# Kernel optimization log

Hardware: AMD Instinct MI355X
Metric: run time of the kernel (lower is better)

The kernel has to match this reference:

```python
import jax, jax.numpy as jnp
import numpy as np

B, S, D, H, DFF = 4, 2048, 2048, 16, 8192
DH = D // H
THETA = 10000.0
EPS = 1e-5


def rmsnorm(x, g):
    return x * jax.lax.rsqrt(jnp.mean(x * x, axis=-1, keepdims=True) + EPS) * g


def rope(x, pos):
    # x: [B, H, S, DH]; rotate interleaved even/odd pairs
    half = DH // 2
    inv_freq = THETA ** (-(jnp.arange(half, dtype=jnp.float32) * 2.0) / DH)  # [half]
    ang = pos.astype(jnp.float32)[:, None] * inv_freq  # [S, half]
    cos, sin = jnp.cos(ang), jnp.sin(ang)
    x1, x2 = x[..., 0::2], x[..., 1::2]
    r1 = x1 * cos - x2 * sin
    r2 = x1 * sin + x2 * cos
    return jnp.stack([r1, r2], axis=-1).reshape(x.shape)


def setup_inputs() -> dict:
    key = jax.random.key(0)
    ks = jax.random.split(key, 12)
    s = 0.02
    return {
        "x": jax.random.normal(ks[0], (B, S, D), dtype=jnp.float32),
        "attention_mask": jnp.ones((S, S), dtype=bool),
        "wq": jax.random.normal(ks[1], (D, D), dtype=jnp.float32) * s,
        "wk": jax.random.normal(ks[2], (D, D), dtype=jnp.float32) * s,
        "wv": jax.random.normal(ks[3], (D, D), dtype=jnp.float32) * s,
        "wo": jax.random.normal(ks[4], (D, D), dtype=jnp.float32) * s,
        "w1": jax.random.normal(ks[5], (DFF, D), dtype=jnp.float32) * s,
        "w2": jax.random.normal(ks[6], (D, DFF), dtype=jnp.float32) * s,
        "w3": jax.random.normal(ks[7], (DFF, D), dtype=jnp.float32) * s,
        "g1": jnp.ones((D,), dtype=jnp.float32),
        "g2": jnp.ones((D,), dtype=jnp.float32),
    }


def reference(x, attention_mask, wq, wk, wv, wo, w1, w2, w3, g1, g2):
    pos = jnp.arange(x.shape[-2])
    # pre-norm attention
    h = rmsnorm(x, g1)
    q = (h @ wq.T).reshape(B, S, H, DH).transpose(0, 2, 1, 3)
    k = (h @ wk.T).reshape(B, S, H, DH).transpose(0, 2, 1, 3)
    v = (h @ wv.T).reshape(B, S, H, DH).transpose(0, 2, 1, 3)
    q = rope(q, pos)
    k = rope(k, pos)
    scores = jnp.einsum("bhqd,bhkd->bhqk", q, k) / np.float32(np.sqrt(DH))
    scores = jnp.where(attention_mask, scores, jnp.float32(-1e9))
    attn = jax.nn.softmax(scores, axis=-1)
    o = jnp.einsum("bhqk,bhkd->bhqd", attn, v)
    o = o.transpose(0, 2, 1, 3).reshape(B, S, D) @ wo.T
    x = x + o
    # pre-norm SwiGLU FFN
    h2 = rmsnorm(x, g2)
    ffn = (jax.nn.silu(h2 @ w1.T) * (h2 @ w3.T)) @ w2.T
    return x + ffn
```

## Files before the change

### kernel.cpp

```cpp
#include <hip/hip_runtime.h>
#include <cstdint>
#include <cstddef>

#define B_   4
#define S_   2048
#define D_   2048
#define H_   16
#define DH_  128
#define DFF_ 8192
#define LOG2E 1.4426950408889634f

typedef __bf16 bf16_t;
typedef __bf16 bf16x4 __attribute__((ext_vector_type(4)));
typedef __bf16 bf16x8 __attribute__((ext_vector_type(8)));
typedef float  f32x4  __attribute__((ext_vector_type(4)));

#define MFMA16 __builtin_amdgcn_mfma_f32_16x16x32_bf16

__device__ __forceinline__ void glds16(const void* g, void* l) {
  __builtin_amdgcn_global_load_lds((__attribute__((address_space(1))) void*)g,
                                   (__attribute__((address_space(3))) void*)l,
                                   16, 0, 0);
}

__global__ __launch_bounds__(256) void cvt_kernel(const float* __restrict__ in,
                                                  bf16_t* __restrict__ out, int n8) {
  int i = blockIdx.x * 256 + threadIdx.x;
  if (i >= n8) return;
  const float4* p4 = (const float4*)in;
  float4 a = p4[2 * (size_t)i];
  float4 b = p4[2 * (size_t)i + 1];
  bf16x8 o;
  o[0] = (bf16_t)a.x; o[1] = (bf16_t)a.y; o[2] = (bf16_t)a.z; o[3] = (bf16_t)a.w;
  o[4] = (bf16_t)b.x; o[5] = (bf16_t)b.y; o[6] = (bf16_t)b.z; o[7] = (bf16_t)b.w;
  ((bf16x8*)out)[i] = o;
}

__global__ __launch_bounds__(256) void rmsnorm_kernel(const float* __restrict__ x,
                                                      const float* __restrict__ g,
                                                      bf16_t* __restrict__ out) {
  const int row = blockIdx.x, tid = threadIdx.x;
  const float* xr = x + (size_t)row * D_;
  float4 a = ((const float4*)xr)[tid * 2];
  float4 b = ((const float4*)xr)[tid * 2 + 1];
  float ss = a.x*a.x + a.y*a.y + a.z*a.z + a.w*a.w
           + b.x*b.x + b.y*b.y + b.z*b.z + b.w*b.w;
#pragma unroll
  for (int m = 1; m < 64; m <<= 1) ss += __shfl_xor(ss, m);
  __shared__ float red[4];
  if ((tid & 63) == 0) red[tid >> 6] = ss;
  __syncthreads();
  float tot = red[0] + red[1] + red[2] + red[3];
  float rms = rsqrtf(tot * (1.0f / D_) + 1e-5f);
  float4 ga = ((const float4*)g)[tid * 2];
  float4 gb = ((const float4*)g)[tid * 2 + 1];
  bf16x8 o;
  o[0] = (bf16_t)(a.x * rms * ga.x); o[1] = (bf16_t)(a.y * rms * ga.y);
  o[2] = (bf16_t)(a.z * rms * ga.z); o[3] = (bf16_t)(a.w * rms * ga.w);
  o[4] = (bf16_t)(b.x * rms * gb.x); o[5] = (bf16_t)(b.y * rms * gb.y);
  o[6] = (bf16_t)(b.z * rms * gb.z); o[7] = (bf16_t)(b.w * rms * gb.w);
  ((bf16x8*)out)[(size_t)row * 256 + tid] = o;
}


#define Q_RD_A(d, mg)                                                         \
  do {                                                                        \
    const char* p_ = ldsb + (d) * 32768 + (wm * 128 + (mg) * 64 + l15) * 128; \
    _Pragma("unroll") for (int i_ = 0; i_ < 4; i_++) {                        \
      afr[i_][0] = *(const bf16x8*)(p_ + i_ * 2048 + acol0);                  \
      afr[i_][1] = *(const bf16x8*)(p_ + i_ * 2048 + acol1);                  \
    }                                                                         \
  } while (0)

#define Q_RD_B(dst, d, ng)                                                    \
  do {                                                                        \
    const char* p_ = ldsb + 65536 + (d) * 32768 +                             \
                     (wn * 64 + (ng) * 32 + l15) * 128;                       \
    _Pragma("unroll") for (int j_ = 0; j_ < 2; j_++) {                        \
      dst[j_][0] = *(const bf16x8*)(p_ + j_ * 2048 + acol0);                  \
      dst[j_][1] = *(const bf16x8*)(p_ + j_ * 2048 + acol1);                  \
    }                                                                         \
  } while (0)

#define Q_STAGE_A(d, kt)                                                      \
  do {                                                                        \
    char* dst_ = ldsb + (d) * 32768 + o0;                                     \
    const bf16_t* s_ = Asrc + (size_t)(kt) * 64;                              \
    glds16(s_, dst_);                                                         \
    glds16(s_ + 64 * (size_t)K, dst_ + 8192);                                 \
    glds16(s_ + 128 * (size_t)K, dst_ + 16384);                               \
    glds16(s_ + 192 * (size_t)K, dst_ + 24576);                               \
  } while (0)

#define Q_STAGE_B(d, kt)                                                      \
  do {                                                                        \
    char* dst_ = ldsb + 65536 + (d) * 32768 + o0;                             \
    const bf16_t* s_ = Wsrc + (size_t)(kt) * 64;                              \
    glds16(s_, dst_);                                                         \
    glds16(s_ + 64 * (size_t)K, dst_ + 8192);                                 \
    glds16(s_ + 128 * (size_t)K, dst_ + 16384);                               \
    glds16(s_ + 192 * (size_t)K, dst_ + 24576);                               \
  } while (0)

#define Q_MFMA(mg, ng, bsrc)                                                  \
  do {                                                                        \
    __builtin_amdgcn_s_setprio(1);                                            \
    _Pragma("unroll") for (int i_ = 0; i_ < 4; i_++)                          \
    _Pragma("unroll") for (int j_ = 0; j_ < 2; j_++) {                        \
      acc[(mg)*4 + i_][(ng)*2 + j_] =                                         \
          MFMA16(afr[i_][0], bsrc[j_][0], acc[(mg)*4 + i_][(ng)*2 + j_], 0,0,0); \
      acc[(mg)*4 + i_][(ng)*2 + j_] =                                         \
          MFMA16(afr[i_][1], bsrc[j_][1], acc[(mg)*4 + i_][(ng)*2 + j_], 0,0,0); \
    }                                                                         \
    __builtin_amdgcn_s_setprio(0);                                            \
  } while (0)

#define Q_MFMA_NS(mg, ng, bsrc)                                               \
  do {                                                                        \
    _Pragma("unroll") for (int i_ = 0; i_ < 4; i_++)                          \
    _Pragma("unroll") for (int j_ = 0; j_ < 2; j_++) {                        \
      acc[(mg)*4 + i_][(ng)*2 + j_] =                                         \
          MFMA16(afr[i_][0], bsrc[j_][0], acc[(mg)*4 + i_][(ng)*2 + j_], 0,0,0); \
      acc[(mg)*4 + i_][(ng)*2 + j_] =                                         \
          MFMA16(afr[i_][1], bsrc[j_][1], acc[(mg)*4 + i_][(ng)*2 + j_], 0,0,0); \
    }                                                                         \
  } while (0)

#define PHASE_FENCE()                                                         \
  do {                                                                        \
    __builtin_amdgcn_sched_barrier(0);                                        \
    __builtin_amdgcn_s_barrier();                                             \
  } while (0)

#define GEMM_EPILOGUE()                                                       \
  _Pragma("unroll") for (int m = 0; m < 8; m++) {                             \
    const int gr = m0 + wm * 128 + m * 16 + lg * 4;                           \
    _Pragma("unroll") for (int nn = 0; nn < 4; nn++) {                        \
      const int gc = n0 + wn * 64 + nn * 16 + l15;                            \
      if constexpr (EPI == 4) {                                               \
        const int seg = gc >> 11;                                             \
        const int gcl = gc & 2047;                                            \
        if (seg < 2) {                                                        \
          bf16_t* o = seg ? outb2 : outb;                                     \
          _Pragma("unroll") for (int r = 0; r < 4; r++)                       \
            o[(size_t)(gr + r) * D_ + gcl] = (bf16_t)acc[m][nn][r];           \
        } else {                                                              \
          const int bb = gr >> 11, ss = gr & 2047;                            \
          bf16x4 pk;                                                          \
          _Pragma("unroll") for (int r = 0; r < 4; r++) pk[r] = (bf16_t)acc[m][nn][r]; \
          *(bf16x4*)(outb3 + ((size_t)bb * D_ + gcl) * S_ + ss) = pk;         \
        }                                                                     \
      } else {                                                                \
        _Pragma("unroll") for (int r = 0; r < 4; r++) {                       \
          size_t idx = (size_t)(gr + r) * N + gc;                             \
          if constexpr (EPI == 0) {                                           \
            outb[idx] = (bf16_t)acc[m][nn][r];                                \
          } else if constexpr (EPI == 1) {                                    \
            outf[idx] = acc[m][nn][r] + addf[idx];                            \
          } else {                                                            \
            float a1v = (float)addb[idx];                                     \
            outb[idx] = (bf16_t)(a1v / (1.0f + expf(-a1v)) * acc[m][nn][r]);  \
          }                                                                   \
        }                                                                     \
      }                                                                       \
    }                                                                         \
  }

#define GEMM_PREAMBLE()                                                       \
  __shared__ char ldsb[131072];                                               \
  const int tid = threadIdx.x;                                                \
  const int wid = tid >> 6, l = tid & 63, l15 = l & 15, lg = l >> 4;          \
  const int wm = wid >> 2, wn = wid & 3;                                      \
  const int nwg = gridDim.x;                                                  \
  int wg = (int)blockIdx.x;                                                   \
  wg = (wg & 7) * (nwg >> 3) + (wg >> 3);                                     \
  const int ntn = N >> 8;                                                     \
  const int m0 = (wg / ntn) << 8, n0 = (wg % ntn) << 8;                       \
  f32x4 acc[8][4];                                                            \
  const f32x4 z4 = {0.f, 0.f, 0.f, 0.f};                                      \
  _Pragma("unroll") for (int i = 0; i < 8; i++)                               \
  _Pragma("unroll") for (int j = 0; j < 4; j++) acc[i][j] = z4;               \
  const int o0 = tid * 16;                                                    \
  const int srow = o0 >> 7;                                                   \
  const int ssw = ((o0 & 127) ^ ((srow & 7) << 4)) >> 1;                      \
  const bf16_t* Asrc = A + (size_t)(m0 + srow) * K + ssw;                     \
  const bf16_t* Wsrc = W + (size_t)(n0 + srow) * K + ssw;                     \
  const int rsw = (l15 & 7) << 4;                                             \
  const int acol0 = (lg * 16) ^ rsw;                                          \
  const int acol1 = (64 + lg * 16) ^ rsw;

template <int EPI>
__global__ __launch_bounds__(512, 2) void gemm256(const bf16_t* __restrict__ A,
                                                  const bf16_t* __restrict__ W,
                                                  const float* __restrict__ addf,
                                                  const bf16_t* __restrict__ addb,
                                                  bf16_t* __restrict__ outb,
                                                  bf16_t* __restrict__ outb2,
                                                  bf16_t* __restrict__ outb3,
                                                  float* __restrict__ outf,
                                                  int M, int N, int K) {
  GEMM_PREAMBLE()
  bf16x8 afr[4][2], bfr[2][2];

  const int NT = K >> 6;
  Q_STAGE_A(0, 0);
  Q_STAGE_B(0, 0);
  asm volatile("s_waitcnt vmcnt(0)" ::: "memory");
  __builtin_amdgcn_s_barrier();

  for (int t = 0; t < NT; t++) {
    const int d = t & 1;
    const bool pf = (t + 1 < NT);
    Q_RD_A(d, 0);
    Q_RD_B(bfr, d, 0);
    if (pf) Q_STAGE_A(d ^ 1, t + 1);
    PHASE_FENCE();
    Q_MFMA(0, 0, bfr);
    PHASE_FENCE();
    Q_RD_B(bfr, d, 1);
    if (pf) Q_STAGE_B(d ^ 1, t + 1);
    PHASE_FENCE();
    Q_MFMA(0, 1, bfr);
    PHASE_FENCE();
    Q_RD_A(d, 1);
    PHASE_FENCE();
    Q_MFMA(1, 1, bfr);
    PHASE_FENCE();
    Q_RD_B(bfr, d, 0);
    PHASE_FENCE();
    Q_MFMA(1, 0, bfr);
    asm volatile("s_waitcnt lgkmcnt(0) vmcnt(0)" ::: "memory");
    __builtin_amdgcn_sched_barrier(0);
    __builtin_amdgcn_s_barrier();
  }

  GEMM_EPILOGUE()
}

template <int EPI>
__global__ __launch_bounds__(512, 1) void gemm256s(const bf16_t* __restrict__ A,
                                                   const bf16_t* __restrict__ W,
                                                   const float* __restrict__ addf,
                                                   const bf16_t* __restrict__ addb,
                                                   bf16_t* __restrict__ outb,
                                                   bf16_t* __restrict__ outb2,
                                                   bf16_t* __restrict__ outb3,
                                                   float* __restrict__ outf,
                                                   int M, int N, int K) {
  GEMM_PREAMBLE()
  bf16x8 afr[4][2], bf0[2][2], bf1[2][2];

  const int NT = K >> 6;
  Q_STAGE_A(0, 0); Q_STAGE_B(0, 0);
  Q_STAGE_A(1, 1); Q_STAGE_B(1, 1);

  for (int t = 0; t < NT; t++) {
    const int d = t & 1;
    if (t + 1 < NT) asm volatile("s_waitcnt vmcnt(8)" ::: "memory");
    else            asm volatile("s_waitcnt vmcnt(0)" ::: "memory");
    __builtin_amdgcn_s_barrier();
    __builtin_amdgcn_sched_barrier(0);
    Q_RD_B(bf0, d, 0);
    Q_RD_A(d, 0);
    Q_MFMA_NS(0, 0, bf0);
    Q_RD_B(bf1, d, 1);
    Q_MFMA_NS(0, 1, bf1);
    Q_RD_A(d, 1);
    Q_MFMA_NS(1, 1, bf1);
    Q_MFMA_NS(1, 0, bf0);
    __builtin_amdgcn_sched_barrier(0);
    __builtin_amdgcn_s_barrier();
    if (t + 2 < NT) { Q_STAGE_A(d, t + 2); Q_STAGE_B(d, t + 2); }
  }

  GEMM_EPILOGUE()
}

__global__ __launch_bounds__(256) void rope_kernel(bf16_t* __restrict__ buf) {
  size_t i = (size_t)blockIdx.x * 256 + threadIdx.x;
  int pi = (int)(i & 63);
  size_t rh = i >> 6;
  int srow = (int)((rh / H_) % S_);
  float inv = expf((float)pi * (-9.210340371976184f / 64.0f));
  float ang = (float)srow * inv;
  float c = cosf(ang), sn = sinf(ang);
  bf16_t* p = buf + i * 2;
  float x1 = (float)p[0], x2 = (float)p[1];
  p[0] = (bf16_t)(x1 * c - x2 * sn);
  p[1] = (bf16_t)(x1 * sn + x2 * c);
}

__global__ __launch_bounds__(256) void attn_kernel(const bf16_t* __restrict__ Q,
                                                   const bf16_t* __restrict__ Kb,
                                                   const bf16_t* __restrict__ Vt,
                                                   bf16_t* __restrict__ O) {
  const int qt = blockIdx.x, h = blockIdx.y, b = blockIdx.z;
  const int tid = threadIdx.x;
  const int wid = tid >> 6, l = tid & 63, l15 = l & 15, lg = l >> 4;

  __shared__ bf16_t Klds[64 * 128];
  __shared__ bf16_t Vlds[128 * 64];
  __shared__ bf16_t Plds[4][16 * 72];

  const int q0 = qt * 64 + wid * 16;
  const f32x4 z4 = {0.f, 0.f, 0.f, 0.f};

  bf16x8 qf[4];
  {
    const bf16_t* qp = Q + ((size_t)(b * S_ + q0 + l15)) * D_ + h * DH_ + lg * 8;
#pragma unroll
    for (int kk = 0; kk < 4; kk++) qf[kk] = *(const bf16x8*)(qp + kk * 32);
  }
  f32x4 of[8];
#pragma unroll
  for (int f = 0; f < 8; f++) of[f] = z4;
  float m_run = -1e30f, l_run = 0.f;

  const int o0 = tid * 16;
  const int krow0 = o0 >> 8;
  const int scol = ((o0 & 255) ^ ((krow0 & 7) << 4)) >> 1;
  const int vrow0 = o0 >> 7;
  const int vcol = ((o0 & 127) ^ ((vrow0 & 7) << 4)) >> 1;

  const size_t bh_off = ((size_t)b * S_) * D_ + (size_t)h * DH_;
  const bf16_t* vtbase = Vt + ((size_t)b * D_ + h * DH_) * S_;

  for (int kv0 = 0; kv0 < S_; kv0 += 64) {
    const bf16_t* kbase = Kb + bh_off + (size_t)kv0 * D_;
#pragma unroll
    for (int s = 0; s < 4; s++)
      glds16(kbase + (size_t)(krow0 + 16 * s) * D_ + scol,
             (char*)Klds + s * 4096 + wid * 1024);
#pragma unroll
    for (int s = 0; s < 4; s++)
      glds16(vtbase + (size_t)(vrow0 + 32 * s) * S_ + kv0 + vcol,
             (char*)Vlds + s * 4096 + wid * 1024);
    __syncthreads();

    f32x4 st[4];
#pragma unroll
    for (int c = 0; c < 4; c++) {
      st[c] = z4;
      const int row = c * 16 + l15;
      const char* kr = (const char*)Klds + row * 256;
      const int sw = (row & 7) << 4;
#pragma unroll
      for (int kk = 0; kk < 4; kk++) {
        bf16x8 kf = *(const bf16x8*)(kr + ((kk * 64 + lg * 16) ^ sw));
        st[c] = MFMA16(kf, qf[kk], st[c], 0, 0, 0);
      }
    }

    float s[16];
#pragma unroll
    for (int c = 0; c < 4; c++)
#pragma unroll
      for (int r = 0; r < 4; r++) s[c * 4 + r] = st[c][r] * 0.08838834764831845f;
    float pm = s[0];
#pragma unroll
    for (int i = 1; i < 16; i++) pm = fmaxf(pm, s[i]);
    pm = fmaxf(pm, __shfl_xor(pm, 16));
    pm = fmaxf(pm, __shfl_xor(pm, 32));
    float mnew = fmaxf(m_run, pm);
    float alpha = exp2f((m_run - mnew) * LOG2E);
    float p[16], ts = 0.f;
#pragma unroll
    for (int i = 0; i < 16; i++) { p[i] = exp2f((s[i] - mnew) * LOG2E); ts += p[i]; }
    ts += __shfl_xor(ts, 16);
    ts += __shfl_xor(ts, 32);
    l_run = l_run * alpha + ts;
    m_run = mnew;

    float aq[4];
#pragma unroll
    for (int r = 0; r < 4; r++) aq[r] = __shfl(alpha, lg * 4 + r);
#pragma unroll
    for (int f = 0; f < 8; f++)
#pragma unroll
      for (int r = 0; r < 4; r++) of[f][r] *= aq[r];

    bf16_t* pw = &Plds[wid][0];
#pragma unroll
    for (int c = 0; c < 4; c++)
#pragma unroll
      for (int r = 0; r < 4; r++)
        pw[l15 * 72 + c * 16 + lg * 4 + r] = (bf16_t)p[c * 4 + r];
    asm volatile("s_waitcnt lgkmcnt(0)" ::: "memory");
    bf16x8 pa0 = *(const bf16x8*)(pw + l15 * 72 + lg * 8);
    bf16x8 pa1 = *(const bf16x8*)(pw + l15 * 72 + 32 + lg * 8);
#pragma unroll
    for (int f = 0; f < 8; f++) {
      const int row = 16 * f + l15;
      const char* vr = (const char*)Vlds + row * 128;
      const int sw = (row & 7) << 4;
      bf16x8 bv0 = *(const bf16x8*)(vr + ((lg * 16) ^ sw));
      bf16x8 bv1 = *(const bf16x8*)(vr + ((64 + lg * 16) ^ sw));
      of[f] = MFMA16(pa0, bv0, of[f], 0, 0, 0);
      of[f] = MFMA16(pa1, bv1, of[f], 0, 0, 0);
    }
    __syncthreads();
  }

  float inv[4];
#pragma unroll
  for (int r = 0; r < 4; r++) inv[r] = 1.0f / __shfl(l_run, lg * 4 + r);
#pragma unroll
  for (int f = 0; f < 8; f++)
#pragma unroll
    for (int r = 0; r < 4; r++)
      O[((size_t)(b * S_ + q0 + lg * 4 + r)) * D_ + h * DH_ + 16 * f + l15] =
          (bf16_t)(of[f][r] * inv[r]);
}

extern "C" void kernel_launch(void* const* d_in, const int* in_sizes, int n_in,
                              void* d_out, int out_size, void* d_ws, size_t ws_size,
                              hipStream_t stream) {
  const float* x  = (const float*)d_in[0];
  const float* wq = (const float*)d_in[2];
  const float* wk = (const float*)d_in[3];
  const float* wv = (const float*)d_in[4];
  const float* wo = (const float*)d_in[5];
  const float* w1 = (const float*)d_in[6];
  const float* w2 = (const float*)d_in[7];
  const float* w3 = (const float*)d_in[8];
  const float* g1 = (const float*)d_in[9];
  const float* g2 = (const float*)d_in[10];
  float* out = (float*)d_out;

  const size_t ND = (size_t)D_ * D_;
  const size_t NF = (size_t)DFF_ * D_;
  const size_t SLOT = NF * 2;
  char* base = (char*)d_ws;
  bf16_t* wslot = (bf16_t*)(base);
  bf16_t* h1    = (bf16_t*)(base + 1 * SLOT);
  bf16_t* qb    = (bf16_t*)(base + 2 * SLOT);
  bf16_t* kb    = (bf16_t*)(base + 3 * SLOT);
  bf16_t* vt    = (bf16_t*)(base + 4 * SLOT);
  bf16_t* ob    = (bf16_t*)(base + 5 * SLOT);
  bf16_t* h2    = h1;
  bf16_t* g     = qb;
  float*  x1    = out;

  auto cvt = [&](const float* in, bf16_t* o, size_t n) {
    int n8 = (int)(n / 8);
    cvt_kernel<<<(n8 + 255) / 256, 256, 0, stream>>>(in, o, n8);
  };

  rmsnorm_kernel<<<B_ * S_, 256, 0, stream>>>(x, g1, h1);

  cvt(wq, wslot, ND);
  cvt(wk, wslot + ND, ND);
  cvt(wv, wslot + 2 * ND, ND);
  const int gqkv3 = (8192 / 256) * (6144 / 256);
  gemm256<4><<<gqkv3, 512, 0, stream>>>(h1, wslot, nullptr, nullptr,
                                        qb, kb, vt, nullptr, 8192, 6144, 2048);

  rope_kernel<<<(B_ * S_ * H_ * 64) / 256, 256, 0, stream>>>(qb);
  rope_kernel<<<(B_ * S_ * H_ * 64) / 256, 256, 0, stream>>>(kb);

  dim3 ga(S_ / 64, H_, B_);
  attn_kernel<<<ga, 256, 0, stream>>>(qb, kb, vt, ob);

  const int gqkv = (8192 / 256) * (2048 / 256);
  cvt(wo, wslot, ND);
  gemm256<1><<<gqkv, 512, 0, stream>>>(ob, wslot, x, nullptr,
                                       nullptr, nullptr, nullptr, x1, 8192, 2048, 2048);

  rmsnorm_kernel<<<B_ * S_, 256, 0, stream>>>(x1, g2, h2);

  const int gff = (8192 / 256) * (8192 / 256);
  cvt(w1, wslot, NF);
  gemm256s<0><<<gff, 512, 0, stream>>>(h2, wslot, nullptr, nullptr,
                                       g, nullptr, nullptr, nullptr, 8192, 8192, 2048);

  cvt(w3, wslot, NF);
  gemm256s<2><<<gff, 512, 0, stream>>>(h2, wslot, nullptr, g,
                                       g, nullptr, nullptr, nullptr, 8192, 8192, 2048);

  cvt(w2, wslot, NF);
  gemm256<1><<<gqkv, 512, 0, stream>>>(g, wslot, x1, nullptr,
                                       nullptr, nullptr, nullptr, x1, 8192, 2048, 8192);
}
```

Baseline: 1.465 ms.

## Use column-band tile ordering and drop the simple gemm256s FFN kernel

```diff
diff --git a/kernel.cpp b/kernel.cpp
--- a/kernel.cpp
+++ b/kernel.cpp
@@ -113,17 +113,6 @@
           MFMA16(afr[i_][1], bsrc[j_][1], acc[(mg)*4 + i_][(ng)*2 + j_], 0,0,0); \
     }                                                                         \
     __builtin_amdgcn_s_setprio(0);                                            \
-  } while (0)
-
-#define Q_MFMA_NS(mg, ng, bsrc)                                               \
-  do {                                                                        \
-    _Pragma("unroll") for (int i_ = 0; i_ < 4; i_++)                          \
-    _Pragma("unroll") for (int j_ = 0; j_ < 2; j_++) {                        \
-      acc[(mg)*4 + i_][(ng)*2 + j_] =                                         \
-          MFMA16(afr[i_][0], bsrc[j_][0], acc[(mg)*4 + i_][(ng)*2 + j_], 0,0,0); \
-      acc[(mg)*4 + i_][(ng)*2 + j_] =                                         \
-          MFMA16(afr[i_][1], bsrc[j_][1], acc[(mg)*4 + i_][(ng)*2 + j_], 0,0,0); \
-    }                                                                         \
   } while (0)
 
 #define PHASE_FENCE()                                                         \
@@ -175,7 +164,12 @@
   int wg = (int)blockIdx.x;                                                   \
   wg = (wg & 7) * (nwg >> 3) + (wg >> 3);                                     \
   const int ntn = N >> 8;                                                     \
-  const int m0 = (wg / ntn) << 8, n0 = (wg % ntn) << 8;                       \
+  const int ntm = M >> 8;                                                     \
+  const int wide = 4 * ntm;                                                   \
+  const int grp = wg / wide;                                                  \
+  const int rem = wg % wide;                                                  \
+  const int m0 = (rem >> 2) << 8;                                             \
+  const int n0 = ((grp << 2) + (rem & 3)) << 8;                               \
   f32x4 acc[8][4];                                                            \
   const f32x4 z4 = {0.f, 0.f, 0.f, 0.f};                                      \
   _Pragma("unroll") for (int i = 0; i < 8; i++)                               \
@@ -232,45 +226,6 @@
     asm volatile("s_waitcnt lgkmcnt(0) vmcnt(0)" ::: "memory");
     __builtin_amdgcn_sched_barrier(0);
     __builtin_amdgcn_s_barrier();
-  }
-
-  GEMM_EPILOGUE()
-}
-
-template <int EPI>
-__global__ __launch_bounds__(512, 1) void gemm256s(const bf16_t* __restrict__ A,
-                                                   const bf16_t* __restrict__ W,
-                                                   const float* __restrict__ addf,
-                                                   const bf16_t* __restrict__ addb,
-                                                   bf16_t* __restrict__ outb,
-                                                   bf16_t* __restrict__ outb2,
-                                                   bf16_t* __restrict__ outb3,
-                                                   float* __restrict__ outf,
-                                                   int M, int N, int K) {
-  GEMM_PREAMBLE()
-  bf16x8 afr[4][2], bf0[2][2], bf1[2][2];
-
-  const int NT = K >> 6;
-  Q_STAGE_A(0, 0); Q_STAGE_B(0, 0);
-  Q_STAGE_A(1, 1); Q_STAGE_B(1, 1);
-
-  for (int t = 0; t < NT; t++) {
-    const int d = t & 1;
-    if (t + 1 < NT) asm volatile("s_waitcnt vmcnt(8)" ::: "memory");
-    else            asm volatile("s_waitcnt vmcnt(0)" ::: "memory");
-    __builtin_amdgcn_s_barrier();
-    __builtin_amdgcn_sched_barrier(0);
-    Q_RD_B(bf0, d, 0);
-    Q_RD_A(d, 0);
-    Q_MFMA_NS(0, 0, bf0);
-    Q_RD_B(bf1, d, 1);
-    Q_MFMA_NS(0, 1, bf1);
-    Q_RD_A(d, 1);
-    Q_MFMA_NS(1, 1, bf1);
-    Q_MFMA_NS(1, 0, bf0);
-    __builtin_amdgcn_sched_barrier(0);
-    __builtin_amdgcn_s_barrier();
-    if (t + 2 < NT) { Q_STAGE_A(d, t + 2); Q_STAGE_B(d, t + 2); }
   }
 
   GEMM_EPILOGUE()
@@ -470,12 +425,12 @@
 
   const int gff = (8192 / 256) * (8192 / 256);
   cvt(w1, wslot, NF);
-  gemm256s<0><<<gff, 512, 0, stream>>>(h2, wslot, nullptr, nullptr,
-                                       g, nullptr, nullptr, nullptr, 8192, 8192, 2048);
+  gemm256<0><<<gff, 512, 0, stream>>>(h2, wslot, nullptr, nullptr,
+                                      g, nullptr, nullptr, nullptr, 8192, 8192, 2048);
 
   cvt(w3, wslot, NF);
-  gemm256s<2><<<gff, 512, 0, stream>>>(h2, wslot, nullptr, g,
-                                       g, nullptr, nullptr, nullptr, 8192, 8192, 2048);
+  gemm256<2><<<gff, 512, 0, stream>>>(h2, wslot, nullptr, g,
+                                      g, nullptr, nullptr, nullptr, 8192, 8192, 2048);
 
   cvt(w2, wslot, NF);
   gemm256<1><<<gqkv, 512, 0, stream>>>(g, wslot, x1, nullptr,
```

Result: no change. 1.437 ms (-1.9%).

## Remap GEMM tile order into column groups and stagger wave MFMA phases

Applied to the files above, without the earlier changes.

```diff
diff --git a/kernel.cpp b/kernel.cpp
--- a/kernel.cpp
+++ b/kernel.cpp
@@ -113,17 +113,6 @@
           MFMA16(afr[i_][1], bsrc[j_][1], acc[(mg)*4 + i_][(ng)*2 + j_], 0,0,0); \
     }                                                                         \
     __builtin_amdgcn_s_setprio(0);                                            \
-  } while (0)
-
-#define Q_MFMA_NS(mg, ng, bsrc)                                               \
-  do {                                                                        \
-    _Pragma("unroll") for (int i_ = 0; i_ < 4; i_++)                          \
-    _Pragma("unroll") for (int j_ = 0; j_ < 2; j_++) {                        \
-      acc[(mg)*4 + i_][(ng)*2 + j_] =                                         \
-          MFMA16(afr[i_][0], bsrc[j_][0], acc[(mg)*4 + i_][(ng)*2 + j_], 0,0,0); \
-      acc[(mg)*4 + i_][(ng)*2 + j_] =                                         \
-          MFMA16(afr[i_][1], bsrc[j_][1], acc[(mg)*4 + i_][(ng)*2 + j_], 0,0,0); \
-    }                                                                         \
   } while (0)
 
 #define PHASE_FENCE()                                                         \
@@ -175,7 +164,12 @@
   int wg = (int)blockIdx.x;                                                   \
   wg = (wg & 7) * (nwg >> 3) + (wg >> 3);                                     \
   const int ntn = N >> 8;                                                     \
-  const int m0 = (wg / ntn) << 8, n0 = (wg % ntn) << 8;                       \
+  const int ntm = M >> 8;                                                     \
+  const int wide = 4 * ntm;                                                   \
+  const int grp = wg / wide;                                                  \
+  const int rem = wg % wide;                                                  \
+  const int m0 = (rem >> 2) << 8;                                             \
+  const int n0 = ((grp << 2) + (rem & 3)) << 8;                               \
   f32x4 acc[8][4];                                                            \
   const f32x4 z4 = {0.f, 0.f, 0.f, 0.f};                                      \
   _Pragma("unroll") for (int i = 0; i < 8; i++)                               \
@@ -238,7 +232,7 @@
 }
 
 template <int EPI>
-__global__ __launch_bounds__(512, 1) void gemm256s(const bf16_t* __restrict__ A,
+__global__ __launch_bounds__(512, 1) void gemm256x(const bf16_t* __restrict__ A,
                                                    const bf16_t* __restrict__ W,
                                                    const float* __restrict__ addf,
                                                    const bf16_t* __restrict__ addb,
@@ -260,14 +254,25 @@
     else            asm volatile("s_waitcnt vmcnt(0)" ::: "memory");
     __builtin_amdgcn_s_barrier();
     __builtin_amdgcn_sched_barrier(0);
-    Q_RD_B(bf0, d, 0);
-    Q_RD_A(d, 0);
-    Q_MFMA_NS(0, 0, bf0);
-    Q_RD_B(bf1, d, 1);
-    Q_MFMA_NS(0, 1, bf1);
-    Q_RD_A(d, 1);
-    Q_MFMA_NS(1, 1, bf1);
-    Q_MFMA_NS(1, 0, bf0);
+    if (wid < 4) {
+      Q_RD_B(bf0, d, 0);
+      Q_RD_A(d, 0);
+      Q_MFMA(0, 0, bf0);
+      Q_RD_B(bf1, d, 1);
+      Q_MFMA(0, 1, bf1);
+      Q_RD_A(d, 1);
+      Q_MFMA(1, 1, bf1);
+      Q_MFMA(1, 0, bf0);
+    } else {
+      Q_RD_B(bf1, d, 1);
+      Q_RD_A(d, 1);
+      Q_MFMA(1, 1, bf1);
+      Q_RD_B(bf0, d, 0);
+      Q_MFMA(1, 0, bf0);
+      Q_RD_A(d, 0);
+      Q_MFMA(0, 0, bf0);
+      Q_MFMA(0, 1, bf1);
+    }
     __builtin_amdgcn_sched_barrier(0);
     __builtin_amdgcn_s_barrier();
     if (t + 2 < NT) { Q_STAGE_A(d, t + 2); Q_STAGE_B(d, t + 2); }
@@ -470,11 +475,11 @@
 
   const int gff = (8192 / 256) * (8192 / 256);
   cvt(w1, wslot, NF);
-  gemm256s<0><<<gff, 512, 0, stream>>>(h2, wslot, nullptr, nullptr,
+  gemm256x<0><<<gff, 512, 0, stream>>>(h2, wslot, nullptr, nullptr,
                                        g, nullptr, nullptr, nullptr, 8192, 8192, 2048);
 
   cvt(w3, wslot, NF);
-  gemm256s<2><<<gff, 512, 0, stream>>>(h2, wslot, nullptr, g,
+  gemm256x<2><<<gff, 512, 0, stream>>>(h2, wslot, nullptr, g,
                                        g, nullptr, nullptr, nullptr, 8192, 8192, 2048);
 
   cvt(w2, wslot, NF);
```

Measured after the change: 1.450 ms. No clear change (-1.0%).
